# Kernel optimization log

Hardware: AMD Instinct MI355X
Metric: run time of the kernel (lower is better)

## Reference

```python
import jax, jax.numpy as jnp
import numpy as np

NEG_SLOPE = 0.2   # RGATConv default negative_slope
BN_EPS = 1e-5     # torch BatchNorm1d default eps


def _build_edges(n0, n1, batch):
    """Replicates generate_edges_union + PyG Batch offsetting. Returns [2, B*E] src/dst and [B*E] edge types."""
    n = n0 + n1
    def perm(k, off):  # itertools.permutations(range(k), 2) as (src, dst) columns
        a = np.repeat(np.arange(k), k); b = np.tile(np.arange(k), k)
        m = a != b
        return np.stack([a[m], b[m]]) + off
    intra = np.concatenate([perm(n0, 0), perm(n1, n0)], axis=1)                 # edge_type 0
    ca = np.repeat(np.arange(n0), n1); cb = np.tile(np.arange(n0, n), n0)
    cross = np.concatenate([np.stack([ca, cb]), np.stack([cb, ca])], axis=1)    # edge_type 1
    edges = np.concatenate([intra, cross], axis=1)
    etype = np.concatenate([np.zeros(intra.shape[1], np.int32), np.ones(cross.shape[1], np.int32)])
    offs = (np.arange(batch) * n)[:, None, None]
    edges_b = (edges[None, :, :] + offs).transpose(1, 0, 2).reshape(2, -1)      # per-graph node offsets
    etype_b = np.tile(etype, batch)
    return jnp.asarray(edges_b, jnp.int32), jnp.asarray(etype_b, jnp.int32)


def _segment_softmax(logits, seg, num_seg):
    m = jax.ops.segment_max(logits, seg, num_segments=num_seg)
    m = jnp.where(jnp.isfinite(m), m, 0.0)
    e = jnp.exp(logits - m[seg])
    s = jax.ops.segment_sum(e, seg, num_segments=num_seg)
    return e / (s[seg] + 1e-16)  # PyG softmax eps


def _rgat_layer(x, src, dst, etype, W, q, k, b, num_nodes):
    # PyG RGATConv: heads=1, dim=1, concat=False, additive-self-attention, across-relation softmax, aggr=add
    H = jnp.einsum('nf,rfe->rne', x, W)            # relation-specific transform: [2, BN, F]
    qs = jnp.einsum('rne,e->rn', H, q)             # q-score per node per relation
    ks = jnp.einsum('rne,e->rn', H, k)
    logit = jax.nn.leaky_relu(qs[etype, dst] + ks[etype, src], NEG_SLOPE)  # [E]
    alpha = _segment_softmax(logit, dst, num_nodes)
    msg = alpha[:, None] * H[etype, src]           # [E, F] per-edge messages
    out = jax.ops.segment_sum(msg, dst, num_segments=num_nodes)
    return out + b                                 # heads=1 -> mean over heads is identity; + bias


def setup_inputs() -> dict:
    key = jax.random.key(0)
    ks = jax.random.split(key, 6)
    B, F, N0, N1, L = 4, 256, 128, 128, 3
    s = 0.05
    return {
        'desc0': jax.random.normal(ks[0], (B, F, N0), jnp.float32),
        'desc1': jax.random.normal(ks[1], (B, F, N1), jnp.float32),
        'conv_w': jax.random.normal(ks[2], (L, 2, F, F), jnp.float32) * s,
        'conv_q': jax.random.normal(ks[3], (L, F), jnp.float32) * s,
        'conv_k': jax.random.normal(ks[4], (L, F), jnp.float32) * s,
        'conv_b': jnp.zeros((L, F), jnp.float32),
        'lin_w': jax.random.normal(ks[5], (L, F, 2 * F), jnp.float32) * s,
        'lin_b': jnp.zeros((L, F), jnp.float32),
        'bn_w': jnp.ones((L, F), jnp.float32),
        'bn_b': jnp.zeros((L, F), jnp.float32),
    }


def reference(desc0, desc1, conv_w, conv_q, conv_k, conv_b, lin_w, lin_b, bn_w, bn_b):
    b, f, n0 = desc0.shape
    n1 = desc1.shape[2]
    n = n0 + n1
    # [B, F, N] -> batched node features [B*N, F]
    x = jnp.concatenate([desc0, desc1], axis=2).transpose(0, 2, 1).reshape(b * n, f)
    edges, etype = _build_edges(n0, n1, b)
    src, dst = edges[0], edges[1]
    num_nodes = b * n
    for i in range(conv_w.shape[0]):
        msg1 = jax.nn.relu(_rgat_layer(x, src, dst, etype, conv_w[i], conv_q[i], conv_k[i], conv_b[i], num_nodes))
        msg2 = jnp.concatenate([x, msg1], axis=1) @ lin_w[i].T + lin_b[i]
        mu = msg2.mean(axis=0)
        var = msg2.var(axis=0)  # biased, as torch BatchNorm uses for normalization (training mode)
        msg3 = bn_w[i] * (msg2 - mu) / jnp.sqrt(var + BN_EPS) + bn_b[i]
        x = x + msg3            # edge_pool[i] == 1 -> no knn_graph rebuild
    x = x.reshape(b, n, f).transpose(0, 2, 1)
    return x[:, :, :n0], x[:, :, n0:]
```

## Files before the change

### kernel.cpp

```cpp
#include <hip/hip_runtime.h>
#include <math.h>


typedef __attribute__((ext_vector_type(8))) short short8;
typedef __attribute__((ext_vector_type(4))) float f32x4;
typedef unsigned short u16;
typedef unsigned int   u32;

__device__ __forceinline__ u16 f2bf(float f) {
    union { float f; u32 u; } v; v.f = f;
    u32 r = v.u + 0x7fffu + ((v.u >> 16) & 1u);
    return (u16)(r >> 16);
}
__device__ __forceinline__ short8 ld8(const u16* p) {
    return __builtin_bit_cast(short8, *(const int4*)p);
}

__global__ __launch_bounds__(256) void k_prep(
    const float* __restrict__ d0, const float* __restrict__ d1,
    const float* __restrict__ conv_w, const float* __restrict__ lin_w,
    float* __restrict__ x, u16* __restrict__ xb,
    u16* __restrict__ Wt, u16* __restrict__ lwb) {
    for (int i = blockIdx.x * 256 + threadIdx.x; i < 1048576; i += 262144) {
        if (i < 262144) {
            int node = i >> 8, f = i & 255, b = node >> 8, nl = node & 255;
            float v = (nl < 128) ? d0[b * 32768 + f * 128 + nl]
                                 : d1[b * 32768 + f * 128 + (nl - 128)];
            x[i] = v; xb[i] = f2bf(v);
        } else if (i < 655360) {
            int o = i - 262144;
            int mat = o >> 16, rem = o & 65535, e = rem >> 8, f = rem & 255;
            Wt[o] = f2bf(conv_w[mat * 65536 + f * 256 + e]);
        } else {
            int o = i - 655360;
            lwb[o] = f2bf(lin_w[o]);
        }
    }
}

__global__ __launch_bounds__(256, 1) void k_hqk(
    const float* __restrict__ xprev, const float* __restrict__ msg2,
    const float* __restrict__ sums, const float* __restrict__ sumsq,
    const float* __restrict__ bw, const float* __restrict__ bb,
    const u16* __restrict__ cwt,
    const float* __restrict__ cq, const float* __restrict__ ck,
    float* __restrict__ xcur, u16* __restrict__ xb, u16* __restrict__ Ht,
    float* __restrict__ qpart, float* __restrict__ kpart, int do_bn) {
    __shared__ __align__(16) u16 Asub[16 * 264];
    const int tid = threadIdx.x;
    const int mt = blockIdx.x >> 2, eg = blockIdx.x & 3;
    const int m0 = mt * 16;
    const int lane = tid & 63, widx = tid >> 6;
    const int row = lane & 15, kg = lane >> 4;

    float scale = 0.f, shift = 0.f;
    if (do_bn) {
        float s1 = 0.f, s2 = 0.f;
        #pragma unroll 8
        for (int c = 0; c < 64; ++c) { s1 += sums[c * 256 + tid]; s2 += sumsq[c * 256 + tid]; }
        float mu  = s1 * (1.f / 1024.f);
        float var = s2 * (1.f / 1024.f) - mu * mu;
        scale = bw[tid] * rsqrtf(var + 1e-5f);
        shift = bb[tid] - mu * scale;
    }
    #pragma unroll
    for (int r = 0; r < 16; ++r) {
        int idx = (m0 + r) * 256 + tid;
        float v = xprev[idx];
        if (do_bn) v += msg2[idx] * scale + shift;
        u16 hb = f2bf(v);
        Asub[r * 264 + tid] = hb;
        if (do_bn && eg == 0) { xcur[idx] = v; xb[idx] = hb; }
    }
    __syncthreads();

    const int et = eg * 4 + widx, e0 = et * 16;
    const u16* B0 = cwt + (e0 + row) * 256 + kg * 8;
    const u16* B1 = B0 + 65536;
    const u16* Ap = &Asub[row * 264 + kg * 8];
    f32x4 acc0 = {0.f,0.f,0.f,0.f}, acc1 = {0.f,0.f,0.f,0.f};
    #pragma unroll
    for (int k0 = 0; k0 < 256; k0 += 32) {
        short8 a = ld8(Ap + k0);
        acc0 = __builtin_amdgcn_mfma_f32_16x16x32_bf16(a, ld8(B0 + k0), acc0, 0, 0, 0);
        acc1 = __builtin_amdgcn_mfma_f32_16x16x32_bf16(a, ld8(B1 + k0), acc1, 0, 0, 0);
    }
    ushort4 o0, o1;
    o0.x = f2bf(acc0[0]); o0.y = f2bf(acc0[1]); o0.z = f2bf(acc0[2]); o0.w = f2bf(acc0[3]);
    o1.x = f2bf(acc1[0]); o1.y = f2bf(acc1[1]); o1.z = f2bf(acc1[2]); o1.w = f2bf(acc1[3]);
    *(ushort4*)(Ht + (e0 + row) * 1024 + m0 + kg * 4) = o0;
    *(ushort4*)(Ht + 262144 + (e0 + row) * 1024 + m0 + kg * 4) = o1;
    float qe = cq[e0 + row], ke = ck[e0 + row];
    float pq0[4], pk0[4], pq1[4], pk1[4];
    #pragma unroll
    for (int c = 0; c < 4; ++c) {
        pq0[c] = acc0[c] * qe; pk0[c] = acc0[c] * ke;
        pq1[c] = acc1[c] * qe; pk1[c] = acc1[c] * ke;
    }
    #pragma unroll
    for (int off = 1; off < 16; off <<= 1) {
        #pragma unroll
        for (int c = 0; c < 4; ++c) {
            pq0[c] += __shfl_xor(pq0[c], off);
            pk0[c] += __shfl_xor(pk0[c], off);
            pq1[c] += __shfl_xor(pq1[c], off);
            pk1[c] += __shfl_xor(pk1[c], off);
        }
    }
    if (row == 0) {
        float4 a4 = {pq0[0], pq0[1], pq0[2], pq0[3]};
        float4 b4 = {pk0[0], pk0[1], pk0[2], pk0[3]};
        float4 c4 = {pq1[0], pq1[1], pq1[2], pq1[3]};
        float4 d4 = {pk1[0], pk1[1], pk1[2], pk1[3]};
        *(float4*)&qpart[et * 1024 + m0 + kg * 4] = a4;
        *(float4*)&kpart[et * 1024 + m0 + kg * 4] = b4;
        *(float4*)&qpart[(16 + et) * 1024 + m0 + kg * 4] = c4;
        *(float4*)&kpart[(16 + et) * 1024 + m0 + kg * 4] = d4;
    }
}

__global__ __launch_bounds__(256, 1) void k_attn(
    const float* __restrict__ qpart, const float* __restrict__ kpart,
    const u16* __restrict__ Ht, const float* __restrict__ cb,
    u16* __restrict__ msg1b) {
    __shared__ __align__(16) u16 Atile[16 * 264];
    __shared__ float ksl[2][256];
    __shared__ float qsl[2][16];
    __shared__ __align__(16) float T[4][16 * 20];
    const int tid = threadIdx.x;
    const int mt = blockIdx.x >> 2, eg = blockIdx.x & 3;
    const int m0 = mt * 16;
    const int g = m0 >> 8, a = (m0 >> 7) & 1;
    {
        float k0s = 0.f, k1s = 0.f;
        #pragma unroll
        for (int c = 0; c < 16; ++c) {
            k0s += kpart[c * 1024 + g * 256 + tid];
            k1s += kpart[(16 + c) * 1024 + g * 256 + tid];
        }
        ksl[0][tid] = k0s; ksl[1][tid] = k1s;
    }
    if (tid < 32) {
        int rel = tid >> 4, r = tid & 15;
        float q = 0.f;
        #pragma unroll
        for (int c = 0; c < 16; ++c) q += qpart[(rel * 16 + c) * 1024 + m0 + r];
        qsl[rel][r] = q;
    }
    __syncthreads();
    {
        const int r = tid >> 4, j = tid & 15;
        const int dl = (m0 + r) & 255;
        const int s0 = j * 16;
        const int rel = ((s0 >> 7) == a) ? 0 : 1;
        float qv = qsl[rel][r];
        float l[16], mx = -1e30f;
        #pragma unroll
        for (int i2 = 0; i2 < 16; ++i2) {
            float v = qv + ksl[rel][s0 + i2];
            v = (v >= 0.f) ? v : 0.2f * v;
            if (s0 + i2 == dl) v = -1e30f;
            l[i2] = v; mx = fmaxf(mx, v);
        }
        #pragma unroll
        for (int off = 1; off < 16; off <<= 1) mx = fmaxf(mx, __shfl_xor(mx, off));
        float s = 0.f;
        #pragma unroll
        for (int i2 = 0; i2 < 16; ++i2) { l[i2] = __expf(l[i2] - mx); s += l[i2]; }
        #pragma unroll
        for (int off = 1; off < 16; off <<= 1) s += __shfl_xor(s, off);
        float inv = 1.f / (s + 1e-16f);
        #pragma unroll
        for (int i2 = 0; i2 < 16; i2 += 2) {
            u32 p = (u32)f2bf(l[i2] * inv) | ((u32)f2bf(l[i2 + 1] * inv) << 16);
            *(u32*)&Atile[r * 264 + s0 + i2] = p;
        }
    }
    __syncthreads();
    const int lane = tid & 63, widx = tid >> 6;
    const int row = lane & 15, kg = lane >> 4;
    const int et = eg * 4 + widx, e0 = et * 16;
    const u16* Ap = &Atile[row * 264 + kg * 8];
    f32x4 acc = {0.f,0.f,0.f,0.f};
    #pragma unroll
    for (int k0 = 0; k0 < 256; k0 += 32) {
        const int rel = (((k0 >> 7) & 1) == a) ? 0 : 1;
        const u16* B = Ht + rel * 262144 + (e0 + row) * 1024 + g * 256 + k0 + kg * 8;
        acc = __builtin_amdgcn_mfma_f32_16x16x32_bf16(ld8(Ap + k0), ld8(B), acc, 0, 0, 0);
    }
    float bias = cb[e0 + row];
    float* Tw = &T[widx][0];
    #pragma unroll
    for (int c = 0; c < 4; ++c)
        Tw[(kg * 4 + c) * 20 + row] = fmaxf(acc[c] + bias, 0.f);
    __syncthreads();
    float4 v = *(float4*)&Tw[row * 20 + kg * 4];
    u32 lo = (u32)f2bf(v.x) | ((u32)f2bf(v.y) << 16);
    u32 hi = (u32)f2bf(v.z) | ((u32)f2bf(v.w) << 16);
    uint2 ov = {lo, hi};
    *(uint2*)(msg1b + (m0 + row) * 256 + e0 + kg * 4) = ov;
}

__global__ __launch_bounds__(256, 1) void k_lin(
    const u16* __restrict__ xb, const u16* __restrict__ msg1b,
    const u16* __restrict__ lwp, const float* __restrict__ lb,
    float* __restrict__ msg2, float* __restrict__ sums, float* __restrict__ sumsq) {
    __shared__ __align__(16) float T[4][16 * 20];
    const int tid = threadIdx.x, lane = tid & 63, widx = tid >> 6;
    const int row = lane & 15, kg = lane >> 4;
    const int mt = blockIdx.x >> 2, ng = blockIdx.x & 3;
    const int m0 = mt * 16;
    const int nt = ng * 4 + widx, n0 = nt * 16;
    const u16* A0 = xb    + (m0 + row) * 256 + kg * 8;
    const u16* A1 = msg1b + (m0 + row) * 256 + kg * 8;
    const u16* B  = lwp + (n0 + row) * 512 + kg * 8;
    f32x4 acc = {0.f,0.f,0.f,0.f};
    #pragma unroll
    for (int k0 = 0; k0 < 512; k0 += 32) {
        short8 av = (k0 < 256) ? ld8(A0 + k0) : ld8(A1 + (k0 - 256));
        acc = __builtin_amdgcn_mfma_f32_16x16x32_bf16(av, ld8(B + k0), acc, 0, 0, 0);
    }
    float bias = lb[n0 + row];
    float v0 = acc[0] + bias, v1 = acc[1] + bias, v2 = acc[2] + bias, v3 = acc[3] + bias;
    float s1 = v0 + v1 + v2 + v3;
    float s2 = v0 * v0 + v1 * v1 + v2 * v2 + v3 * v3;
    s1 += __shfl_xor(s1, 16); s1 += __shfl_xor(s1, 32);
    s2 += __shfl_xor(s2, 16); s2 += __shfl_xor(s2, 32);
    if (lane < 16) {
        sums [mt * 256 + n0 + lane] = s1;
        sumsq[mt * 256 + n0 + lane] = s2;
    }
    float* Tw = &T[widx][0];
    Tw[(kg * 4 + 0) * 20 + row] = v0;
    Tw[(kg * 4 + 1) * 20 + row] = v1;
    Tw[(kg * 4 + 2) * 20 + row] = v2;
    Tw[(kg * 4 + 3) * 20 + row] = v3;
    __syncthreads();
    float4 vv = *(float4*)&Tw[row * 20 + kg * 4];
    *(float4*)(msg2 + (m0 + row) * 256 + n0 + kg * 4) = vv;
}

__global__ __launch_bounds__(256) void k_fin(
    const float* __restrict__ x2, const float* __restrict__ msg2,
    const float* __restrict__ sums, const float* __restrict__ sumsq,
    const float* __restrict__ bw, const float* __restrict__ bb,
    float* __restrict__ out) {
    const int blk = blockIdx.x, t = threadIdx.x;
    float s1 = 0.f, s2 = 0.f;
    #pragma unroll 8
    for (int c = 0; c < 64; ++c) { s1 += sums[c * 256 + t]; s2 += sumsq[c * 256 + t]; }
    float mu  = s1 * (1.f / 1024.f);
    float var = s2 * (1.f / 1024.f) - mu * mu;
    float scale = bw[t] * rsqrtf(var + 1e-5f);
    float shift = bb[t] - mu * scale;
    #pragma unroll
    for (int j = 0; j < 4; ++j) {
        int node = blk * 4 + j;
        int idx = node * 256 + t;
        float v = x2[idx] + msg2[idx] * scale + shift;
        int b = node >> 8, nl = node & 255, half = nl >> 7, n = nl & 127;
        out[half * 131072 + b * 32768 + t * 128 + n] = v;
    }
}

extern "C" void kernel_launch(void* const* d_in, const int* in_sizes, int n_in,
                              void* d_out, int out_size, void* d_ws, size_t ws_size,
                              hipStream_t stream) {
    const float* desc0  = (const float*)d_in[0];
    const float* desc1  = (const float*)d_in[1];
    const float* conv_w = (const float*)d_in[2];
    const float* conv_q = (const float*)d_in[3];
    const float* conv_k = (const float*)d_in[4];
    const float* conv_b = (const float*)d_in[5];
    const float* lin_w  = (const float*)d_in[6];
    const float* lin_b  = (const float*)d_in[7];
    const float* bn_w   = (const float*)d_in[8];
    const float* bn_b   = (const float*)d_in[9];
    float* out = (float*)d_out;

    char* p = (char*)d_ws;
    float* x0     = (float*)p; p += 1048576;
    float* x1     = (float*)p; p += 1048576;
    u16*   xb     = (u16*)p;   p += 524288;
    u16*   Wt     = (u16*)p;   p += 786432;
    u16*   lwb    = (u16*)p;   p += 786432;
    u16*   Ht     = (u16*)p;   p += 1048576;
    float* qpart  = (float*)p; p += 131072;
    float* kpart  = (float*)p; p += 131072;
    u16*   msg1b  = (u16*)p;   p += 524288;
    float* msg2   = (float*)p; p += 1048576;
    float* sums   = (float*)p; p += 65536;
    float* sumsq  = (float*)p; p += 65536;

    k_prep<<<1024, 256, 0, stream>>>(desc0, desc1, conv_w, lin_w, x0, xb, Wt, lwb);

    float* xs[4] = {x0, x0, x1, x0};
    for (int i = 0; i < 3; ++i) {
        const u16*   cwt = Wt + i * 131072;
        const u16*   lwp = lwb + i * 131072;
        const float* cq = conv_q + i * 256;
        const float* ck = conv_k + i * 256;
        const float* cb = conv_b + i * 256;
        const float* lb = lin_b + i * 256;
        const float* bwp = bn_w + (i ? (i - 1) * 256 : 0);
        const float* bbp = bn_b + (i ? (i - 1) * 256 : 0);

        k_hqk<<<256, 256, 0, stream>>>(xs[i], msg2, sums, sumsq, bwp, bbp,
                                       cwt, cq, ck, xs[i + 1], xb, Ht,
                                       qpart, kpart, i > 0 ? 1 : 0);
        k_attn<<<256, 256, 0, stream>>>(qpart, kpart, Ht, cb, msg1b);
        k_lin<<<256, 256, 0, stream>>>(xb, msg1b, lwp, lb, msg2, sums, sumsq);
    }

    k_fin<<<256, 256, 0, stream>>>(xs[3], msg2, sums, sumsq,
                                   bn_w + 512, bn_b + 512, out);
}
```

Before: 156.9 us.

## Fuse attention and linear kernels; precompute W·q and W·k projections

Precomputes W·q and W·k per layer and relation in the prep kernel, so attention scores are computed directly from fp32 node features. This removes the per-tile partial-sum buffers and their reduction in the attention kernel. The attention aggregation and the linear+BN-stats kernels are merged into one kernel that keeps msg1 in shared memory, which removes a launch and the global round-trip of msg1. In exchange, the fused kernel runs only 64 larger blocks, which reduces parallelism across the device.

```diff
diff --git a/kernel.cpp b/kernel.cpp
--- a/kernel.cpp
+++ b/kernel.cpp
@@ -19,9 +19,10 @@
 __global__ __launch_bounds__(256) void k_prep(
     const float* __restrict__ d0, const float* __restrict__ d1,
     const float* __restrict__ conv_w, const float* __restrict__ lin_w,
+    const float* __restrict__ conv_q, const float* __restrict__ conv_k,
     float* __restrict__ x, u16* __restrict__ xb,
-    u16* __restrict__ Wt, u16* __restrict__ lwb) {
-    for (int i = blockIdx.x * 256 + threadIdx.x; i < 1048576; i += 262144) {
+    u16* __restrict__ Wt, u16* __restrict__ lwb, float* __restrict__ wqk) {
+    for (int i = blockIdx.x * 256 + threadIdx.x; i < 1051648; i += 262144) {
         if (i < 262144) {
             int node = i >> 8, f = i & 255, b = node >> 8, nl = node & 255;
             float v = (nl < 128) ? d0[b * 32768 + f * 128 + nl]
@@ -31,9 +32,23 @@
             int o = i - 262144;
             int mat = o >> 16, rem = o & 65535, e = rem >> 8, f = rem & 255;
             Wt[o] = f2bf(conv_w[mat * 65536 + f * 256 + e]);
-        } else {
+        } else if (i < 1048576) {
             int o = i - 655360;
             lwb[o] = f2bf(lin_w[o]);
+        } else {
+            int o = i - 1048576;
+            int c2 = o >> 8;
+            int layer = c2 >> 2, rel = (c2 >> 1) & 1, qk = c2 & 1, f = o & 255;
+            const float* vec  = (qk ? conv_k : conv_q) + layer * 256;
+            const float* wrow = conv_w + (layer * 2 + rel) * 65536 + f * 256;
+            float s = 0.f;
+            #pragma unroll 4
+            for (int e = 0; e < 256; e += 4) {
+                float4 w4 = *(const float4*)&wrow[e];
+                float4 v4 = *(const float4*)&vec[e];
+                s += w4.x * v4.x + w4.y * v4.y + w4.z * v4.z + w4.w * v4.w;
+            }
+            wqk[layer * 1024 + (rel * 2 + qk) * 256 + f] = s;
         }
     }
 }
@@ -43,10 +58,12 @@
     const float* __restrict__ sums, const float* __restrict__ sumsq,
     const float* __restrict__ bw, const float* __restrict__ bb,
     const u16* __restrict__ cwt,
-    const float* __restrict__ cq, const float* __restrict__ ck,
+    const float* __restrict__ wqk_l,
     float* __restrict__ xcur, u16* __restrict__ xb, u16* __restrict__ Ht,
-    float* __restrict__ qpart, float* __restrict__ kpart, int do_bn) {
+    float* __restrict__ qkbuf,
+    int do_bn) {
     __shared__ __align__(16) u16 Asub[16 * 264];
+    __shared__ __align__(16) float Xs[16 * 260];
     const int tid = threadIdx.x;
     const int mt = blockIdx.x >> 2, eg = blockIdx.x & 3;
     const int m0 = mt * 16;
@@ -70,6 +87,7 @@
         if (do_bn) v += msg2[idx] * scale + shift;
         u16 hb = f2bf(v);
         Asub[r * 264 + tid] = hb;
+        Xs[r * 260 + tid] = v;
         if (do_bn && eg == 0) { xcur[idx] = v; xb[idx] = hb; }
     }
     __syncthreads();
@@ -90,65 +108,49 @@
     o1.x = f2bf(acc1[0]); o1.y = f2bf(acc1[1]); o1.z = f2bf(acc1[2]); o1.w = f2bf(acc1[3]);
     *(ushort4*)(Ht + (e0 + row) * 1024 + m0 + kg * 4) = o0;
     *(ushort4*)(Ht + 262144 + (e0 + row) * 1024 + m0 + kg * 4) = o1;
-    float qe = cq[e0 + row], ke = ck[e0 + row];
-    float pq0[4], pk0[4], pq1[4], pk1[4];
-    #pragma unroll
-    for (int c = 0; c < 4; ++c) {
-        pq0[c] = acc0[c] * qe; pk0[c] = acc0[c] * ke;
-        pq1[c] = acc1[c] * qe; pk1[c] = acc1[c] * ke;
-    }
-    #pragma unroll
-    for (int off = 1; off < 16; off <<= 1) {
-        #pragma unroll
-        for (int c = 0; c < 4; ++c) {
-            pq0[c] += __shfl_xor(pq0[c], off);
-            pk0[c] += __shfl_xor(pk0[c], off);
-            pq1[c] += __shfl_xor(pq1[c], off);
-            pk1[c] += __shfl_xor(pk1[c], off);
-        }
-    }
-    if (row == 0) {
-        float4 a4 = {pq0[0], pq0[1], pq0[2], pq0[3]};
-        float4 b4 = {pk0[0], pk0[1], pk0[2], pk0[3]};
-        float4 c4 = {pq1[0], pq1[1], pq1[2], pq1[3]};
-        float4 d4 = {pk1[0], pk1[1], pk1[2], pk1[3]};
-        *(float4*)&qpart[et * 1024 + m0 + kg * 4] = a4;
-        *(float4*)&kpart[et * 1024 + m0 + kg * 4] = b4;
-        *(float4*)&qpart[(16 + et) * 1024 + m0 + kg * 4] = c4;
-        *(float4*)&kpart[(16 + et) * 1024 + m0 + kg * 4] = d4;
-    }
-}
-
-__global__ __launch_bounds__(256, 1) void k_attn(
-    const float* __restrict__ qpart, const float* __restrict__ kpart,
-    const u16* __restrict__ Ht, const float* __restrict__ cb,
-    u16* __restrict__ msg1b) {
+
+    if (eg == 0) {
+        const float* wv = wqk_l + widx * 256;
+        float4 w4 = *(const float4*)&wv[lane * 4];
+        #pragma unroll
+        for (int r = 0; r < 16; ++r) {
+            float4 xv = *(const float4*)&Xs[r * 260 + lane * 4];
+            float s = xv.x * w4.x + xv.y * w4.y + xv.z * w4.z + xv.w * w4.w;
+            s += __shfl_xor(s, 32); s += __shfl_xor(s, 16); s += __shfl_xor(s, 8);
+            s += __shfl_xor(s, 4);  s += __shfl_xor(s, 2);  s += __shfl_xor(s, 1);
+            if (lane == 0) qkbuf[widx * 1024 + m0 + r] = s;
+        }
+    }
+}
+
+__global__ __launch_bounds__(512, 1) void k_al(
+    const float* __restrict__ qkbuf, const u16* __restrict__ Ht,
+    const float* __restrict__ cb,
+    const u16* __restrict__ xb, const u16* __restrict__ lwp,
+    const float* __restrict__ lb,
+    float* __restrict__ msg2, float* __restrict__ sums, float* __restrict__ sumsq) {
     __shared__ __align__(16) u16 Atile[16 * 264];
+    __shared__ __align__(16) u16 M1[16 * 264];
     __shared__ float ksl[2][256];
     __shared__ float qsl[2][16];
-    __shared__ __align__(16) float T[4][16 * 20];
+    __shared__ __align__(16) float T[8][16 * 20];
     const int tid = threadIdx.x;
-    const int mt = blockIdx.x >> 2, eg = blockIdx.x & 3;
+    const int mt = blockIdx.x;
     const int m0 = mt * 16;
-    const int g = m0 >> 8, a = (m0 >> 7) & 1;
+    const int g = mt >> 4, a = (mt >> 3) & 1;
+    const int lane = tid & 63, w = tid >> 6;
+    const int row = lane & 15, kg = lane >> 4;
+
     {
-        float k0s = 0.f, k1s = 0.f;
-        #pragma unroll
-        for (int c = 0; c < 16; ++c) {
-            k0s += kpart[c * 1024 + g * 256 + tid];
-            k1s += kpart[(16 + c) * 1024 + g * 256 + tid];
-        }
-        ksl[0][tid] = k0s; ksl[1][tid] = k1s;
+        int rel = tid >> 8, s = tid & 255;
+        ksl[rel][s] = qkbuf[(rel * 2 + 1) * 1024 + g * 256 + s];
     }
     if (tid < 32) {
         int rel = tid >> 4, r = tid & 15;
-        float q = 0.f;
-        #pragma unroll
-        for (int c = 0; c < 16; ++c) q += qpart[(rel * 16 + c) * 1024 + m0 + r];
-        qsl[rel][r] = q;
+        qsl[rel][r] = qkbuf[(rel * 2) * 1024 + m0 + r];
     }
     __syncthreads();
-    {
+    if (tid < 256) {
         const int r = tid >> 4, j = tid & 15;
         const int dl = (m0 + r) & 255;
         const int s0 = j * 16;
@@ -177,67 +179,53 @@
         }
     }
     __syncthreads();
-    const int lane = tid & 63, widx = tid >> 6;
-    const int row = lane & 15, kg = lane >> 4;
-    const int et = eg * 4 + widx, e0 = et * 16;
     const u16* Ap = &Atile[row * 264 + kg * 8];
-    f32x4 acc = {0.f,0.f,0.f,0.f};
-    #pragma unroll
-    for (int k0 = 0; k0 < 256; k0 += 32) {
-        const int rel = (((k0 >> 7) & 1) == a) ? 0 : 1;
-        const u16* B = Ht + rel * 262144 + (e0 + row) * 1024 + g * 256 + k0 + kg * 8;
-        acc = __builtin_amdgcn_mfma_f32_16x16x32_bf16(ld8(Ap + k0), ld8(B), acc, 0, 0, 0);
-    }
-    float bias = cb[e0 + row];
-    float* Tw = &T[widx][0];
-    #pragma unroll
-    for (int c = 0; c < 4; ++c)
-        Tw[(kg * 4 + c) * 20 + row] = fmaxf(acc[c] + bias, 0.f);
+    #pragma unroll
+    for (int it = 0; it < 2; ++it) {
+        const int e0 = (w + it * 8) * 16;
+        f32x4 acc = {0.f,0.f,0.f,0.f};
+        #pragma unroll
+        for (int k0 = 0; k0 < 256; k0 += 32) {
+            const int rel = (((k0 >> 7) & 1) == a) ? 0 : 1;
+            const u16* B = Ht + rel * 262144 + (e0 + row) * 1024 + g * 256 + k0 + kg * 8;
+            acc = __builtin_amdgcn_mfma_f32_16x16x32_bf16(ld8(Ap + k0), ld8(B), acc, 0, 0, 0);
+        }
+        float bias = cb[e0 + row];
+        #pragma unroll
+        for (int c = 0; c < 4; ++c)
+            M1[(kg * 4 + c) * 264 + e0 + row] = f2bf(fmaxf(acc[c] + bias, 0.f));
+    }
     __syncthreads();
-    float4 v = *(float4*)&Tw[row * 20 + kg * 4];
-    u32 lo = (u32)f2bf(v.x) | ((u32)f2bf(v.y) << 16);
-    u32 hi = (u32)f2bf(v.z) | ((u32)f2bf(v.w) << 16);
-    uint2 ov = {lo, hi};
-    *(uint2*)(msg1b + (m0 + row) * 256 + e0 + kg * 4) = ov;
-}
-
-__global__ __launch_bounds__(256, 1) void k_lin(
-    const u16* __restrict__ xb, const u16* __restrict__ msg1b,
-    const u16* __restrict__ lwp, const float* __restrict__ lb,
-    float* __restrict__ msg2, float* __restrict__ sums, float* __restrict__ sumsq) {
-    __shared__ __align__(16) float T[4][16 * 20];
-    const int tid = threadIdx.x, lane = tid & 63, widx = tid >> 6;
-    const int row = lane & 15, kg = lane >> 4;
-    const int mt = blockIdx.x >> 2, ng = blockIdx.x & 3;
-    const int m0 = mt * 16;
-    const int nt = ng * 4 + widx, n0 = nt * 16;
-    const u16* A0 = xb    + (m0 + row) * 256 + kg * 8;
-    const u16* A1 = msg1b + (m0 + row) * 256 + kg * 8;
-    const u16* B  = lwp + (n0 + row) * 512 + kg * 8;
-    f32x4 acc = {0.f,0.f,0.f,0.f};
-    #pragma unroll
-    for (int k0 = 0; k0 < 512; k0 += 32) {
-        short8 av = (k0 < 256) ? ld8(A0 + k0) : ld8(A1 + (k0 - 256));
-        acc = __builtin_amdgcn_mfma_f32_16x16x32_bf16(av, ld8(B + k0), acc, 0, 0, 0);
-    }
-    float bias = lb[n0 + row];
-    float v0 = acc[0] + bias, v1 = acc[1] + bias, v2 = acc[2] + bias, v3 = acc[3] + bias;
-    float s1 = v0 + v1 + v2 + v3;
-    float s2 = v0 * v0 + v1 * v1 + v2 * v2 + v3 * v3;
-    s1 += __shfl_xor(s1, 16); s1 += __shfl_xor(s1, 32);
-    s2 += __shfl_xor(s2, 16); s2 += __shfl_xor(s2, 32);
-    if (lane < 16) {
-        sums [mt * 256 + n0 + lane] = s1;
-        sumsq[mt * 256 + n0 + lane] = s2;
-    }
-    float* Tw = &T[widx][0];
-    Tw[(kg * 4 + 0) * 20 + row] = v0;
-    Tw[(kg * 4 + 1) * 20 + row] = v1;
-    Tw[(kg * 4 + 2) * 20 + row] = v2;
-    Tw[(kg * 4 + 3) * 20 + row] = v3;
-    __syncthreads();
-    float4 vv = *(float4*)&Tw[row * 20 + kg * 4];
-    *(float4*)(msg2 + (m0 + row) * 256 + n0 + kg * 4) = vv;
+    #pragma unroll
+    for (int it = 0; it < 2; ++it) {
+        const int n0 = (w + it * 8) * 16;
+        const u16* A0 = xb + (m0 + row) * 256 + kg * 8;
+        const u16* A1 = &M1[row * 264 + kg * 8];
+        const u16* B  = lwp + (n0 + row) * 512 + kg * 8;
+        f32x4 acc = {0.f,0.f,0.f,0.f};
+        #pragma unroll
+        for (int k0 = 0; k0 < 512; k0 += 32) {
+            short8 av = (k0 < 256) ? ld8(A0 + k0) : ld8(A1 + (k0 - 256));
+            acc = __builtin_amdgcn_mfma_f32_16x16x32_bf16(av, ld8(B + k0), acc, 0, 0, 0);
+        }
+        float bias = lb[n0 + row];
+        float v0 = acc[0] + bias, v1 = acc[1] + bias, v2 = acc[2] + bias, v3 = acc[3] + bias;
+        float s1 = v0 + v1 + v2 + v3;
+        float s2 = v0 * v0 + v1 * v1 + v2 * v2 + v3 * v3;
+        s1 += __shfl_xor(s1, 16); s1 += __shfl_xor(s1, 32);
+        s2 += __shfl_xor(s2, 16); s2 += __shfl_xor(s2, 32);
+        if (lane < 16) {
+            sums [mt * 256 + n0 + lane] = s1;
+            sumsq[mt * 256 + n0 + lane] = s2;
+        }
+        float* Tw = &T[w][0];
+        Tw[(kg * 4 + 0) * 20 + row] = v0;
+        Tw[(kg * 4 + 1) * 20 + row] = v1;
+        Tw[(kg * 4 + 2) * 20 + row] = v2;
+        Tw[(kg * 4 + 3) * 20 + row] = v3;
+        float4 vv = *(float4*)&Tw[row * 20 + kg * 4];
+        *(float4*)(msg2 + (m0 + row) * 256 + n0 + kg * 4) = vv;
+    }
 }
 
 __global__ __launch_bounds__(256) void k_fin(
@@ -285,31 +273,29 @@
     u16*   Wt     = (u16*)p;   p += 786432;
     u16*   lwb    = (u16*)p;   p += 786432;
     u16*   Ht     = (u16*)p;   p += 1048576;
-    float* qpart  = (float*)p; p += 131072;
-    float* kpart  = (float*)p; p += 131072;
-    u16*   msg1b  = (u16*)p;   p += 524288;
+    float* wqk    = (float*)p; p += 12288;
+    float* qkbuf  = (float*)p; p += 16384;
     float* msg2   = (float*)p; p += 1048576;
     float* sums   = (float*)p; p += 65536;
     float* sumsq  = (float*)p; p += 65536;
 
-    k_prep<<<1024, 256, 0, stream>>>(desc0, desc1, conv_w, lin_w, x0, xb, Wt, lwb);
+    k_prep<<<1024, 256, 0, stream>>>(desc0, desc1, conv_w, lin_w, conv_q, conv_k,
+                                     x0, xb, Wt, lwb, wqk);
 
     float* xs[4] = {x0, x0, x1, x0};
     for (int i = 0; i < 3; ++i) {
         const u16*   cwt = Wt + i * 131072;
         const u16*   lwp = lwb + i * 131072;
-        const float* cq = conv_q + i * 256;
-        const float* ck = conv_k + i * 256;
         const float* cb = conv_b + i * 256;
         const float* lb = lin_b + i * 256;
         const float* bwp = bn_w + (i ? (i - 1) * 256 : 0);
         const float* bbp = bn_b + (i ? (i - 1) * 256 : 0);
 
         k_hqk<<<256, 256, 0, stream>>>(xs[i], msg2, sums, sumsq, bwp, bbp,
-                                       cwt, cq, ck, xs[i + 1], xb, Ht,
-                                       qpart, kpart, i > 0 ? 1 : 0);
-        k_attn<<<256, 256, 0, stream>>>(qpart, kpart, Ht, cb, msg1b);
-        k_lin<<<256, 256, 0, stream>>>(xb, msg1b, lwp, lb, msg2, sums, sumsq);
+                                       cwt, wqk + i * 1024, xs[i + 1], xb, Ht,
+                                       qkbuf, i > 0 ? 1 : 0);
+        k_al<<<64, 512, 0, stream>>>(qkbuf, Ht, cb, xb, lwp, lb,
+                                     msg2, sums, sumsq);
     }
 
     k_fin<<<256, 256, 0, stream>>>(xs[3], msg2, sums, sumsq,
```

Result: slower. 190.9 us (+21.7%).

## Fuse attention aggregation and linear/BN-stats kernels via shared-memory msg1 tile

Applied to the files above, without the earlier changes.

Merges k_attn and k_lin into one kernel, k_al. Each block now computes the full 16x256 msg1 tile (four N-tiles per wave) into shared memory, then runs the concat-linear GEMM from it. This removes one launch per layer and the global msg1b round-trip. In exchange each block does four times the attention-GEMM work that was previously split across four blocks, so the attention part is computed redundantly four times, each time reading Ht from global memory.

```diff
diff --git a/kernel.cpp b/kernel.cpp
--- a/kernel.cpp
+++ b/kernel.cpp
@@ -119,18 +119,24 @@
     }
 }
 
-__global__ __launch_bounds__(256, 1) void k_attn(
+__global__ __launch_bounds__(256, 1) void k_al(
     const float* __restrict__ qpart, const float* __restrict__ kpart,
     const u16* __restrict__ Ht, const float* __restrict__ cb,
-    u16* __restrict__ msg1b) {
+    const u16* __restrict__ xb, const u16* __restrict__ lwp,
+    const float* __restrict__ lb,
+    float* __restrict__ msg2, float* __restrict__ sums, float* __restrict__ sumsq) {
     __shared__ __align__(16) u16 Atile[16 * 264];
+    __shared__ __align__(16) u16 M1[16 * 264];
     __shared__ float ksl[2][256];
     __shared__ float qsl[2][16];
     __shared__ __align__(16) float T[4][16 * 20];
     const int tid = threadIdx.x;
-    const int mt = blockIdx.x >> 2, eg = blockIdx.x & 3;
+    const int mt = blockIdx.x >> 2, ng = blockIdx.x & 3;
     const int m0 = mt * 16;
-    const int g = m0 >> 8, a = (m0 >> 7) & 1;
+    const int g = mt >> 4, a = (mt >> 3) & 1;
+    const int lane = tid & 63, w = tid >> 6;
+    const int row = lane & 15, kg = lane >> 4;
+
     {
         float k0s = 0.f, k1s = 0.f;
         #pragma unroll
@@ -177,67 +183,52 @@
         }
     }
     __syncthreads();
-    const int lane = tid & 63, widx = tid >> 6;
-    const int row = lane & 15, kg = lane >> 4;
-    const int et = eg * 4 + widx, e0 = et * 16;
     const u16* Ap = &Atile[row * 264 + kg * 8];
-    f32x4 acc = {0.f,0.f,0.f,0.f};
-    #pragma unroll
-    for (int k0 = 0; k0 < 256; k0 += 32) {
-        const int rel = (((k0 >> 7) & 1) == a) ? 0 : 1;
-        const u16* B = Ht + rel * 262144 + (e0 + row) * 1024 + g * 256 + k0 + kg * 8;
-        acc = __builtin_amdgcn_mfma_f32_16x16x32_bf16(ld8(Ap + k0), ld8(B), acc, 0, 0, 0);
-    }
-    float bias = cb[e0 + row];
-    float* Tw = &T[widx][0];
-    #pragma unroll
-    for (int c = 0; c < 4; ++c)
-        Tw[(kg * 4 + c) * 20 + row] = fmaxf(acc[c] + bias, 0.f);
+    #pragma unroll
+    for (int it = 0; it < 4; ++it) {
+        const int e0 = (w * 4 + it) * 16;
+        f32x4 acc = {0.f,0.f,0.f,0.f};
+        #pragma unroll
+        for (int k0 = 0; k0 < 256; k0 += 32) {
+            const int rel = (((k0 >> 7) & 1) == a) ? 0 : 1;
+            const u16* B = Ht + rel * 262144 + (e0 + row) * 1024 + g * 256 + k0 + kg * 8;
+            acc = __builtin_amdgcn_mfma_f32_16x16x32_bf16(ld8(Ap + k0), ld8(B), acc, 0, 0, 0);
+        }
+        float bias = cb[e0 + row];
+        #pragma unroll
+        for (int c = 0; c < 4; ++c)
+            M1[(kg * 4 + c) * 264 + e0 + row] = f2bf(fmaxf(acc[c] + bias, 0.f));
+    }
     __syncthreads();
-    float4 v = *(float4*)&Tw[row * 20 + kg * 4];
-    u32 lo = (u32)f2bf(v.x) | ((u32)f2bf(v.y) << 16);
-    u32 hi = (u32)f2bf(v.z) | ((u32)f2bf(v.w) << 16);
-    uint2 ov = {lo, hi};
-    *(uint2*)(msg1b + (m0 + row) * 256 + e0 + kg * 4) = ov;
-}
-
-__global__ __launch_bounds__(256, 1) void k_lin(
-    const u16* __restrict__ xb, const u16* __restrict__ msg1b,
-    const u16* __restrict__ lwp, const float* __restrict__ lb,
-    float* __restrict__ msg2, float* __restrict__ sums, float* __restrict__ sumsq) {
-    __shared__ __align__(16) float T[4][16 * 20];
-    const int tid = threadIdx.x, lane = tid & 63, widx = tid >> 6;
-    const int row = lane & 15, kg = lane >> 4;
-    const int mt = blockIdx.x >> 2, ng = blockIdx.x & 3;
-    const int m0 = mt * 16;
-    const int nt = ng * 4 + widx, n0 = nt * 16;
-    const u16* A0 = xb    + (m0 + row) * 256 + kg * 8;
-    const u16* A1 = msg1b + (m0 + row) * 256 + kg * 8;
-    const u16* B  = lwp + (n0 + row) * 512 + kg * 8;
-    f32x4 acc = {0.f,0.f,0.f,0.f};
-    #pragma unroll
-    for (int k0 = 0; k0 < 512; k0 += 32) {
-        short8 av = (k0 < 256) ? ld8(A0 + k0) : ld8(A1 + (k0 - 256));
-        acc = __builtin_amdgcn_mfma_f32_16x16x32_bf16(av, ld8(B + k0), acc, 0, 0, 0);
-    }
-    float bias = lb[n0 + row];
-    float v0 = acc[0] + bias, v1 = acc[1] + bias, v2 = acc[2] + bias, v3 = acc[3] + bias;
-    float s1 = v0 + v1 + v2 + v3;
-    float s2 = v0 * v0 + v1 * v1 + v2 * v2 + v3 * v3;
-    s1 += __shfl_xor(s1, 16); s1 += __shfl_xor(s1, 32);
-    s2 += __shfl_xor(s2, 16); s2 += __shfl_xor(s2, 32);
-    if (lane < 16) {
-        sums [mt * 256 + n0 + lane] = s1;
-        sumsq[mt * 256 + n0 + lane] = s2;
-    }
-    float* Tw = &T[widx][0];
-    Tw[(kg * 4 + 0) * 20 + row] = v0;
-    Tw[(kg * 4 + 1) * 20 + row] = v1;
-    Tw[(kg * 4 + 2) * 20 + row] = v2;
-    Tw[(kg * 4 + 3) * 20 + row] = v3;
-    __syncthreads();
-    float4 vv = *(float4*)&Tw[row * 20 + kg * 4];
-    *(float4*)(msg2 + (m0 + row) * 256 + n0 + kg * 4) = vv;
+    {
+        const int n0 = ng * 64 + w * 16;
+        const u16* A0 = xb + (m0 + row) * 256 + kg * 8;
+        const u16* A1 = &M1[row * 264 + kg * 8];
+        const u16* B  = lwp + (n0 + row) * 512 + kg * 8;
+        f32x4 acc = {0.f,0.f,0.f,0.f};
+        #pragma unroll
+        for (int k0 = 0; k0 < 512; k0 += 32) {
+            short8 av = (k0 < 256) ? ld8(A0 + k0) : ld8(A1 + (k0 - 256));
+            acc = __builtin_amdgcn_mfma_f32_16x16x32_bf16(av, ld8(B + k0), acc, 0, 0, 0);
+        }
+        float bias = lb[n0 + row];
+        float v0 = acc[0] + bias, v1 = acc[1] + bias, v2 = acc[2] + bias, v3 = acc[3] + bias;
+        float s1 = v0 + v1 + v2 + v3;
+        float s2 = v0 * v0 + v1 * v1 + v2 * v2 + v3 * v3;
+        s1 += __shfl_xor(s1, 16); s1 += __shfl_xor(s1, 32);
+        s2 += __shfl_xor(s2, 16); s2 += __shfl_xor(s2, 32);
+        if (lane < 16) {
+            sums [mt * 256 + n0 + lane] = s1;
+            sumsq[mt * 256 + n0 + lane] = s2;
+        }
+        float* Tw = &T[w][0];
+        Tw[(kg * 4 + 0) * 20 + row] = v0;
+        Tw[(kg * 4 + 1) * 20 + row] = v1;
+        Tw[(kg * 4 + 2) * 20 + row] = v2;
+        Tw[(kg * 4 + 3) * 20 + row] = v3;
+        float4 vv = *(float4*)&Tw[row * 20 + kg * 4];
+        *(float4*)(msg2 + (m0 + row) * 256 + n0 + kg * 4) = vv;
+    }
 }
 
 __global__ __launch_bounds__(256) void k_fin(
@@ -287,7 +278,6 @@
     u16*   Ht     = (u16*)p;   p += 1048576;
     float* qpart  = (float*)p; p += 131072;
     float* kpart  = (float*)p; p += 131072;
-    u16*   msg1b  = (u16*)p;   p += 524288;
     float* msg2   = (float*)p; p += 1048576;
     float* sums   = (float*)p; p += 65536;
     float* sumsq  = (float*)p; p += 65536;
@@ -308,8 +298,8 @@
         k_hqk<<<256, 256, 0, stream>>>(xs[i], msg2, sums, sumsq, bwp, bbp,
                                        cwt, cq, ck, xs[i + 1], xb, Ht,
                                        qpart, kpart, i > 0 ? 1 : 0);
-        k_attn<<<256, 256, 0, stream>>>(qpart, kpart, Ht, cb, msg1b);
-        k_lin<<<256, 256, 0, stream>>>(xb, msg1b, lwp, lb, msg2, sums, sumsq);
+        k_al<<<256, 256, 0, stream>>>(qpart, kpart, Ht, cb, xb, lwp, lb,
+                                      msg2, sums, sumsq);
     }
 
     k_fin<<<256, 256, 0, stream>>>(xs[3], msg2, sums, sumsq,
```

After: 168.0 us. 1.07x slower.
